# Kernel optimization log

Measured on AMD Instinct MI355X. Metric: run time of the kernel, lower is better.

## Reference

```python
import jax, jax.numpy as jnp
import numpy as np
from jax import lax

K = 3            # kernel size
KP = K * K       # kernel_size_prod
CENTER = KP // 2 # center tap index
PIXEL_SIZE = 1.0
DILATION = 1


def _unfold(x):
    # torch F.unfold equivalent: [N, C*KP, oh, ow] with channel-major, spatial-minor tap order
    return lax.conv_general_dilated_patches(
        x, filter_shape=(K, K), window_strides=(1, 1),
        padding=((1, 1), (1, 1)), rhs_dilation=(DILATION, DILATION))


def setup_inputs() -> dict:
    key = jax.random.key(0)
    ks = jax.random.split(key, 6)
    N, C, O, H, W = 8, 128, 128, 64, 64
    x = jax.random.normal(ks[0], (N, C, H, W), jnp.float32)
    depth = jax.random.uniform(ks[1], (N, 1, H, W), jnp.float32)  # >0 almost surely
    fx = jax.random.uniform(ks[2], (N,), jnp.float32) + 0.5       # per-image focal scale
    s = 1.0 / np.sqrt(C * KP)
    w0 = jax.random.normal(ks[3], (O, C, K, K), jnp.float32) * s
    w1 = jax.random.normal(ks[4], (O, C, K, K), jnp.float32) * s
    w2 = jax.random.normal(ks[5], (O, C, K, K), jnp.float32) * s
    return {"x": x, "depth": depth, "fx": fx, "w0": w0, "w1": w1, "w2": w2}


def reference(x, depth, fx, w0, w1, w2):
    N, C, H, W = x.shape
    O = w0.shape[0]
    patches = _unfold(x)                      # [N, C*9, oh, ow]
    oh, ow = patches.shape[2], patches.shape[3]
    L = oh * ow
    x_col = patches.reshape(N, C, KP, L)       # [N, C, 9, L]
    d_col = _unfold(depth).reshape(N, KP, L)   # [N, 9, L]

    valid = (d_col != 0.0).astype(jnp.float32)
    valid = valid * valid[:, CENTER:CENTER + 1, :]
    d_col = d_col * valid
    center = d_col[:, CENTER:CENTER + 1, :]    # [N, 1, L]
    grid = PIXEL_SIZE * DILATION * center / fx[:, None, None]
    half = grid * 0.5

    m0 = (jnp.abs(d_col - (center + grid)) <= half).astype(jnp.float32)
    m1 = (jnp.abs(d_col - center) <= half).astype(jnp.float32)
    m1 = jnp.clip(m1 + 1.0 - valid, 0.0, 1.0)
    m2 = (jnp.abs(d_col - (center - grid)) <= half).astype(jnp.float32)

    def branch(w, m):
        # (O, C*9) @ (N, C*9, L) as an einsum over (C, tap)
        return jnp.einsum('ock,nckl->nol', w.reshape(O, C, KP), x_col * m[:, None])

    out = branch(w0, m0) + branch(w1, m1) + branch(w2, m2)
    return out.reshape(N, O, oh, ow)
```

## Files before the change

### kernel.cpp

```cpp
#include <hip/hip_runtime.h>
#include <hip/hip_bf16.h>
#include <cstdint>
#include <cstddef>

#define Nn 8
#define Cc 128
#define Oo 128
#define Hh 64
#define Ww 64
#define LL (Hh * Ww)
#define KP 9

typedef __attribute__((ext_vector_type(8))) short short8;
typedef __attribute__((ext_vector_type(4))) float floatx4;
typedef __attribute__((ext_vector_type(4))) int intx4;

#define SGB(m, s, i) __builtin_amdgcn_sched_group_barrier(m, s, i)

__device__ __forceinline__ unsigned short f2bf(float f) {
  unsigned int u = __float_as_uint(f);
  u += 0x7fffu + ((u >> 16) & 1u);
  return (unsigned short)(u >> 16);
}

__global__ __launch_bounds__(256) void prep_all(const float* __restrict__ x,
                                                const float* __restrict__ w0,
                                                const float* __restrict__ w1,
                                                const float* __restrict__ w2,
                                                unsigned short* __restrict__ xt,
                                                unsigned short* __restrict__ wt2) {
  __shared__ float tile[Cc][Ww + 1];
  __shared__ unsigned short wl[Cc * KP];
  const int bid = blockIdx.x;
  const int t = threadIdx.x;
  if (bid < Nn * Hh) {
    const int n = bid >> 6;
    const int h = bid & 63;
    const float* src = x + (size_t)n * Cc * LL + (size_t)h * Ww;
#pragma unroll
    for (int it = 0; it < 8; ++it) {
      const int idx = t + it * 256;
      const int c = idx >> 4;
      const int w4 = (idx & 15) << 2;
      const float4 v = *reinterpret_cast<const float4*>(src + (size_t)c * LL + w4);
      tile[c][w4 + 0] = v.x; tile[c][w4 + 1] = v.y;
      tile[c][w4 + 2] = v.z; tile[c][w4 + 3] = v.w;
    }
    __syncthreads();
    unsigned short* dst = xt + (size_t)((n * Hh + h) * Ww) * Cc;
#pragma unroll
    for (int it = 0; it < 4; ++it) {
      const int idx = t + it * 256;
      const int w = idx >> 4;
      const int ch = (idx & 15) << 3;
      short8 v;
#pragma unroll
      for (int q = 0; q < 8; ++q)
        ((unsigned short*)&v)[q] = f2bf(tile[ch + q][w]);
      *reinterpret_cast<short8*>(dst + (size_t)w * Cc + ch) = v;
    }
  } else {
    const int bo = bid - Nn * Hh;
    const int b = bo >> 7;
    const int o = bo & 127;
    const float* w = (b == 0) ? w0 : (b == 1) ? w1 : w2;
    const float* src = w + (size_t)o * Cc * KP;
#pragma unroll
    for (int it = 0; it < 5; ++it) {
      const int idx = t + it * 256;
      if (idx < Cc * KP) wl[idx] = f2bf(src[idx]);
    }
    __syncthreads();
    const int obase = ((o >> 6) & 1) * 2048 + ((o >> 5) & 1) * 1024 +
                      ((o >> 4) & 1) * 512 + (o & 15) * 32;
#pragma unroll
    for (int it = 0; it < 5; ++it) {
      const int idx = t + it * 256;
      if (idx < Cc * KP) {
        const int kk = idx >> 7;
        const int c = idx & 127;
        const int c0 = c >> 5;
        const int cc = c & 31;
        wt2[(size_t)(b * 36 + kk * 4 + c0) * 4096 + obase + cc] = wl[c * KP + kk];
      }
    }
  }
}

#define LDXC 132
#define HALO_COLS 66
#define HALO_ROWS 4
#define NSTEP 36
#define BSTRIDE 147456

__global__ __launch_bounds__(256, 2) void conv_main(
    const unsigned short* __restrict__ xt,
    const unsigned short* __restrict__ wt2,
    const float* __restrict__ depth,
    const float* __restrict__ fx,
    float* __restrict__ out) {
  __shared__ unsigned short Xs[HALO_ROWS * HALO_COLS * LDXC];
  __shared__ unsigned int code32[128];

  const int g = blockIdx.x;
  const int n = g >> 6;
  const int rem = g & 63;
  const int pb = rem >> 1;
  const int ob1 = rem & 1;
  const int h0 = pb * 2;

  const int tid = threadIdx.x;
  const int lane = tid & 63;
  const int wave = tid >> 6;
  const int ln15 = lane & 15;
  const int quad = lane >> 4;
  const int hsel = wave >> 1;
  const int m_half = hsel * 64;
  const int wc = wave & 1;

  const unsigned short* wfrag = wt2 + (size_t)(ob1 * 2048 + wc * 1024 + ln15 * 32 + quad * 8);

  short8 Bb[4][6];
  short8 Aa[2][4];

#define LOADB(S)                                                                  \
  if ((S) < NSTEP) {                                                              \
    const unsigned short* bp = wfrag + (size_t)(S) * 4096;                        \
    Bb[(S) & 3][0] = *reinterpret_cast<const short8*>(bp);                        \
    Bb[(S) & 3][1] = *reinterpret_cast<const short8*>(bp + 512);                  \
    Bb[(S) & 3][2] = *reinterpret_cast<const short8*>(bp + BSTRIDE);              \
    Bb[(S) & 3][3] = *reinterpret_cast<const short8*>(bp + BSTRIDE + 512);        \
    Bb[(S) & 3][4] = *reinterpret_cast<const short8*>(bp + 2 * BSTRIDE);          \
    Bb[(S) & 3][5] = *reinterpret_cast<const short8*>(bp + 2 * BSTRIDE + 512);    \
  }

#define LOADA(S)                                                                  \
  if ((S) < NSTEP) {                                                              \
    const int kkp = (S) >> 2, c0p = (S) & 3;                                      \
    const int dyp = kkp / 3, dxp = kkp % 3;                                       \
    const int ab = ((hsel + dyp) * HALO_COLS + ln15 + dxp) * LDXC + quad * 8 + c0p * 32; \
    Aa[(S) & 1][0] = *reinterpret_cast<const short8*>(&Xs[ab]);                   \
    Aa[(S) & 1][1] = *reinterpret_cast<const short8*>(&Xs[ab + 16 * LDXC]);       \
    Aa[(S) & 1][2] = *reinterpret_cast<const short8*>(&Xs[ab + 32 * LDXC]);       \
    Aa[(S) & 1][3] = *reinterpret_cast<const short8*>(&Xs[ab + 48 * LDXC]);       \
  }

  LOADB(0)
  LOADB(1)
  LOADB(2)

#pragma unroll
  for (int it = 0; it < 17; ++it) {
    const int idx = tid + it * 256;
    if (idx < HALO_ROWS * HALO_COLS * 16) {
      const int ch = (idx & 15) << 3;
      const int pixidx = idx >> 4;
      const int lc = pixidx % HALO_COLS;
      const int hrel = pixidx / HALO_COLS;
      const int hh = h0 - 1 + hrel;
      const int ww = lc - 1;
      short8 v = {0, 0, 0, 0, 0, 0, 0, 0};
      if (hh >= 0 && hh < Hh && ww >= 0 && ww < Ww)
        v = *reinterpret_cast<const short8*>(
            xt + (size_t)((n * Hh + hh) * Ww + ww) * Cc + ch);
      *reinterpret_cast<short8*>(&Xs[pixidx * LDXC + ch]) = v;
    }
  }

  if (tid < 128) {
    const int m = tid;
    const int h = h0 + (m >> 6);
    const int w = m & 63;
    const float center = depth[n * LL + h * Ww + w];
    const float fxv = fx[n];
    const float grid = center / fxv;
    const float half = 0.5f * grid;
    unsigned int packed = 0u;
#pragma unroll
    for (int kk = 0; kk < KP; ++kk) {
      const int hh = h + kk / 3 - 1;
      const int ww = w + kk % 3 - 1;
      float d = 0.0f;
      if (hh >= 0 && hh < Hh && ww >= 0 && ww < Ww) d = depth[n * LL + hh * Ww + ww];
      const float valid = (d != 0.0f && center != 0.0f) ? 1.0f : 0.0f;
      const float dm = d * valid;
      unsigned int cb = 0u;
      if (fabsf(dm - (center + grid)) <= half) cb |= 1u;
      float m1v = (fabsf(dm - center) <= half) ? 1.0f : 0.0f;
      m1v = m1v + 1.0f - valid;
      if (m1v > 1.0f) m1v = 1.0f;
      if (m1v > 0.5f) cb |= 2u;
      if (fabsf(dm - (center - grid)) <= half) cb |= 4u;
      packed |= cb << (3 * kk);
    }
    code32[m] = packed;
  }

  __syncthreads();

  unsigned int cd[4];
#pragma unroll
  for (int i = 0; i < 4; ++i) cd[i] = code32[m_half + i * 16 + ln15];

  const floatx4 zf4 = {0.f, 0.f, 0.f, 0.f};
  floatx4 acc[4][2];
#pragma unroll
  for (int i = 0; i < 4; ++i)
#pragma unroll
    for (int j = 0; j < 2; ++j) acc[i][j] = zf4;

  LOADA(0)

#pragma unroll
  for (int s = 0; s < NSTEP; ++s) {
    LOADB(s + 3)
    LOADA(s + 1)
    const int kk = s >> 2;
    const int shift = 3 * kk;
    const short8* B = Bb[s & 3];
    const short8* A = Aa[s & 1];
#pragma unroll
    for (int b = 0; b < 3; ++b) {
#pragma unroll
      for (int i = 0; i < 4; ++i) {
        const int msk = __builtin_amdgcn_sbfe((int)cd[i], shift + b, 1);
        intx4 a4 = *reinterpret_cast<const intx4*>(&A[i]);
        intx4 m4 = {msk, msk, msk, msk};
        a4 &= m4;
        const short8 af = *reinterpret_cast<const short8*>(&a4);
        acc[i][0] = __builtin_amdgcn_mfma_f32_16x16x32_bf16(af, B[b * 2 + 0], acc[i][0], 0, 0, 0);
        acc[i][1] = __builtin_amdgcn_mfma_f32_16x16x32_bf16(af, B[b * 2 + 1], acc[i][1], 0, 0, 0);
      }
    }
    SGB(0x020, 2, 0); SGB(0x008, 4, 0);
    SGB(0x100, 2, 0); SGB(0x008, 4, 0);
    SGB(0x020, 2, 0); SGB(0x008, 4, 0);
    SGB(0x100, 2, 0); SGB(0x008, 4, 0);
    SGB(0x020, 2, 0); SGB(0x008, 8, 0);
  }

#pragma unroll
  for (int i = 0; i < 4; ++i) {
    const int m = m_half + i * 16 + quad * 4;
    const int h = h0 + (m >> 6);
    const int w = m & 63;
#pragma unroll
    for (int j = 0; j < 2; ++j) {
      const int o = ob1 * 64 + wc * 32 + j * 16 + ln15;
      float* dst = out + (size_t)(n * Oo + o) * LL + h * Ww + w;
      *reinterpret_cast<floatx4*>(dst) = acc[i][j];
    }
  }
}

extern "C" void kernel_launch(void* const* d_in, const int* in_sizes, int n_in,
                              void* d_out, int out_size, void* d_ws, size_t ws_size,
                              hipStream_t stream) {
  const float* x     = (const float*)d_in[0];
  const float* depth = (const float*)d_in[1];
  const float* fx    = (const float*)d_in[2];
  const float* w0    = (const float*)d_in[3];
  const float* w1    = (const float*)d_in[4];
  const float* w2    = (const float*)d_in[5];
  float* out = (float*)d_out;

  unsigned short* xt = (unsigned short*)d_ws;
  unsigned short* wt2 = xt + (size_t)Nn * Hh * Ww * Cc;

  prep_all<<<Nn * Hh + 3 * Oo, 256, 0, stream>>>(x, w0, w1, w2, xt, wt2);
  conv_main<<<512, 256, 0, stream>>>(xt, wt2, depth, fx, out);
}
```

Before: 117.6 us.

## Split K across waves with LDS reduction and precompute depth mask codes in prep

Moves the per-pixel depth mask code computation from conv_main into extra blocks of the prep kernel, writing packed codes to workspace. conv_main changes its wave decomposition: each wave now covers all 128 pixels of the tile and half of the channel reduction (split-K), which halves the B-fragment loads per wave and doubles A reuse. The two K halves are summed through LDS before the store. The cost is more accumulator registers (16 floatx4), an extra barrier, and an LDS reduction pass.

```diff
diff --git a/kernel.cpp b/kernel.cpp
--- a/kernel.cpp
+++ b/kernel.cpp
@@ -27,8 +27,11 @@
                                                 const float* __restrict__ w0,
                                                 const float* __restrict__ w1,
                                                 const float* __restrict__ w2,
+                                                const float* __restrict__ depth,
+                                                const float* __restrict__ fx,
                                                 unsigned short* __restrict__ xt,
-                                                unsigned short* __restrict__ wt2) {
+                                                unsigned short* __restrict__ wt2,
+                                                unsigned int* __restrict__ codesg) {
   __shared__ float tile[Cc][Ww + 1];
   __shared__ unsigned short wl[Cc * KP];
   const int bid = blockIdx.x;
@@ -59,7 +62,7 @@
         ((unsigned short*)&v)[q] = f2bf(tile[ch + q][w]);
       *reinterpret_cast<short8*>(dst + (size_t)w * Cc + ch) = v;
     }
-  } else {
+  } else if (bid < Nn * Hh + 3 * Oo) {
     const int bo = bid - Nn * Hh;
     const int b = bo >> 7;
     const int o = bo & 127;
@@ -84,23 +87,49 @@
         wt2[(size_t)(b * 36 + kk * 4 + c0) * 4096 + obase + cc] = wl[c * KP + kk];
       }
     }
+  } else {
+    const int p = (bid - (Nn * Hh + 3 * Oo)) * 256 + t;
+    const int n = p >> 12;
+    const int rem = p & 4095;
+    const int h = rem >> 6;
+    const int w = rem & 63;
+    const float center = depth[p];
+    const float grid = center / fx[n];
+    const float half = 0.5f * grid;
+    unsigned int packed = 0u;
+#pragma unroll
+    for (int kk = 0; kk < KP; ++kk) {
+      const int hh = h + kk / 3 - 1;
+      const int ww = w + kk % 3 - 1;
+      float d = 0.0f;
+      if (hh >= 0 && hh < Hh && ww >= 0 && ww < Ww) d = depth[(n << 12) + hh * Ww + ww];
+      const float valid = (d != 0.0f && center != 0.0f) ? 1.0f : 0.0f;
+      const float dm = d * valid;
+      unsigned int cb = 0u;
+      if (fabsf(dm - (center + grid)) <= half) cb |= 1u;
+      float m1v = (fabsf(dm - center) <= half) ? 1.0f : 0.0f;
+      m1v = m1v + 1.0f - valid;
+      if (m1v > 1.0f) m1v = 1.0f;
+      if (m1v > 0.5f) cb |= 2u;
+      if (fabsf(dm - (center - grid)) <= half) cb |= 4u;
+      packed |= cb << (3 * kk);
+    }
+    codesg[p] = packed;
   }
 }
 
 #define LDXC 132
 #define HALO_COLS 66
 #define HALO_ROWS 4
-#define NSTEP 36
+#define NSTEP 18
 #define BSTRIDE 147456
 
 __global__ __launch_bounds__(256, 2) void conv_main(
     const unsigned short* __restrict__ xt,
     const unsigned short* __restrict__ wt2,
-    const float* __restrict__ depth,
-    const float* __restrict__ fx,
+    const unsigned int* __restrict__ codesg,
     float* __restrict__ out) {
-  __shared__ unsigned short Xs[HALO_ROWS * HALO_COLS * LDXC];
-  __shared__ unsigned int code32[128];
+  __shared__ __align__(16) unsigned short Xs[HALO_ROWS * HALO_COLS * LDXC];
 
   const int g = blockIdx.x;
   const int n = g >> 6;
@@ -114,40 +143,60 @@
   const int wave = tid >> 6;
   const int ln15 = lane & 15;
   const int quad = lane >> 4;
-  const int hsel = wave >> 1;
-  const int m_half = hsel * 64;
   const int wc = wave & 1;
-
-  const unsigned short* wfrag = wt2 + (size_t)(ob1 * 2048 + wc * 1024 + ln15 * 32 + quad * 8);
-
-  short8 Bb[4][6];
-  short8 Aa[2][4];
-
-#define LOADB(S)                                                                  \
-  if ((S) < NSTEP) {                                                              \
-    const unsigned short* bp = wfrag + (size_t)(S) * 4096;                        \
-    Bb[(S) & 3][0] = *reinterpret_cast<const short8*>(bp);                        \
-    Bb[(S) & 3][1] = *reinterpret_cast<const short8*>(bp + 512);                  \
-    Bb[(S) & 3][2] = *reinterpret_cast<const short8*>(bp + BSTRIDE);              \
-    Bb[(S) & 3][3] = *reinterpret_cast<const short8*>(bp + BSTRIDE + 512);        \
-    Bb[(S) & 3][4] = *reinterpret_cast<const short8*>(bp + 2 * BSTRIDE);          \
-    Bb[(S) & 3][5] = *reinterpret_cast<const short8*>(bp + 2 * BSTRIDE + 512);    \
-  }
-
-#define LOADA(S)                                                                  \
-  if ((S) < NSTEP) {                                                              \
-    const int kkp = (S) >> 2, c0p = (S) & 3;                                      \
+  const int ks = wave >> 1;
+
+  const unsigned short* wfragk =
+      wt2 + (size_t)(ob1 * 2048 + wc * 1024 + ln15 * 32 + quad * 8) + (size_t)ks * 8192;
+  const int xbase = quad * 8 + ks * 64;
+
+  short8 Bb[3][6];
+  short8 Aa[2][8];
+
+#define LOADB(SLOT, S)                                                            \
+  {                                                                               \
+    const unsigned short* bp = wfragk + (size_t)((((S) >> 1) * 4) + ((S) & 1)) * 4096; \
+    Bb[SLOT][0] = *reinterpret_cast<const short8*>(bp);                           \
+    Bb[SLOT][1] = *reinterpret_cast<const short8*>(bp + 512);                     \
+    Bb[SLOT][2] = *reinterpret_cast<const short8*>(bp + BSTRIDE);                 \
+    Bb[SLOT][3] = *reinterpret_cast<const short8*>(bp + BSTRIDE + 512);           \
+    Bb[SLOT][4] = *reinterpret_cast<const short8*>(bp + 2 * BSTRIDE);             \
+    Bb[SLOT][5] = *reinterpret_cast<const short8*>(bp + 2 * BSTRIDE + 512);       \
+  }
+
+#define LOADA(SLOT, S)                                                            \
+  {                                                                               \
+    const int kkp = (S) >> 1;                                                     \
     const int dyp = kkp / 3, dxp = kkp % 3;                                       \
-    const int ab = ((hsel + dyp) * HALO_COLS + ln15 + dxp) * LDXC + quad * 8 + c0p * 32; \
-    Aa[(S) & 1][0] = *reinterpret_cast<const short8*>(&Xs[ab]);                   \
-    Aa[(S) & 1][1] = *reinterpret_cast<const short8*>(&Xs[ab + 16 * LDXC]);       \
-    Aa[(S) & 1][2] = *reinterpret_cast<const short8*>(&Xs[ab + 32 * LDXC]);       \
-    Aa[(S) & 1][3] = *reinterpret_cast<const short8*>(&Xs[ab + 48 * LDXC]);       \
-  }
-
-  LOADB(0)
-  LOADB(1)
-  LOADB(2)
+    _Pragma("unroll")                                                             \
+    for (int i = 0; i < 8; ++i) {                                                 \
+      const int off = (((i >> 2) + dyp) * HALO_COLS + (i & 3) * 16 + dxp) * LDXC  \
+                      + ((S) & 1) * 32;                                           \
+      Aa[SLOT][i] = *reinterpret_cast<const short8*>(&Xs[(ln15 + off) * 1 + xbase \
+                      + off - off + (ln15 * 0) + ((((i >> 2) + dyp) * HALO_COLS + (i & 3) * 16 + dxp + ln15) * LDXC + ((S) & 1) * 32 + xbase) - (ln15 + off + xbase)]); \
+    }                                                                             \
+  }
+#undef LOADA
+#define LOADA(SLOT, S)                                                            \
+  {                                                                               \
+    const int kkp = (S) >> 1;                                                     \
+    const int dyp = kkp / 3, dxp = kkp % 3;                                       \
+    _Pragma("unroll")                                                             \
+    for (int i = 0; i < 8; ++i) {                                                 \
+      const int pix = ((i >> 2) + dyp) * HALO_COLS + (i & 3) * 16 + ln15 + dxp;   \
+      Aa[SLOT][i] = *reinterpret_cast<const short8*>(&Xs[pix * LDXC + ((S) & 1) * 32 + xbase]); \
+    }                                                                             \
+  }
+
+  LOADB(0, 0)
+  LOADB(1, 1)
+
+  unsigned int cd[8];
+  {
+    const unsigned int* cp = codesg + (n << 12) + h0 * 64 + ln15;
+#pragma unroll
+    for (int i = 0; i < 8; ++i) cd[i] = cp[i * 16];
+  }
 
 #pragma unroll
   for (int it = 0; it < 17; ++it) {
@@ -167,62 +216,29 @@
     }
   }
 
-  if (tid < 128) {
-    const int m = tid;
-    const int h = h0 + (m >> 6);
-    const int w = m & 63;
-    const float center = depth[n * LL + h * Ww + w];
-    const float fxv = fx[n];
-    const float grid = center / fxv;
-    const float half = 0.5f * grid;
-    unsigned int packed = 0u;
-#pragma unroll
-    for (int kk = 0; kk < KP; ++kk) {
-      const int hh = h + kk / 3 - 1;
-      const int ww = w + kk % 3 - 1;
-      float d = 0.0f;
-      if (hh >= 0 && hh < Hh && ww >= 0 && ww < Ww) d = depth[n * LL + hh * Ww + ww];
-      const float valid = (d != 0.0f && center != 0.0f) ? 1.0f : 0.0f;
-      const float dm = d * valid;
-      unsigned int cb = 0u;
-      if (fabsf(dm - (center + grid)) <= half) cb |= 1u;
-      float m1v = (fabsf(dm - center) <= half) ? 1.0f : 0.0f;
-      m1v = m1v + 1.0f - valid;
-      if (m1v > 1.0f) m1v = 1.0f;
-      if (m1v > 0.5f) cb |= 2u;
-      if (fabsf(dm - (center - grid)) <= half) cb |= 4u;
-      packed |= cb << (3 * kk);
-    }
-    code32[m] = packed;
-  }
-
   __syncthreads();
 
-  unsigned int cd[4];
-#pragma unroll
-  for (int i = 0; i < 4; ++i) cd[i] = code32[m_half + i * 16 + ln15];
-
   const floatx4 zf4 = {0.f, 0.f, 0.f, 0.f};
-  floatx4 acc[4][2];
-#pragma unroll
-  for (int i = 0; i < 4; ++i)
+  floatx4 acc[8][2];
+#pragma unroll
+  for (int i = 0; i < 8; ++i)
 #pragma unroll
     for (int j = 0; j < 2; ++j) acc[i][j] = zf4;
 
-  LOADA(0)
+  LOADA(0, 0)
 
 #pragma unroll
   for (int s = 0; s < NSTEP; ++s) {
-    LOADB(s + 3)
-    LOADA(s + 1)
-    const int kk = s >> 2;
+    if (s + 2 < NSTEP) LOADB((s + 2) % 3, s + 2)
+    if (s + 1 < NSTEP) LOADA((s + 1) & 1, s + 1)
+    const int kk = s >> 1;
     const int shift = 3 * kk;
-    const short8* B = Bb[s & 3];
+    const short8* B = Bb[s % 3];
     const short8* A = Aa[s & 1];
 #pragma unroll
     for (int b = 0; b < 3; ++b) {
 #pragma unroll
-      for (int i = 0; i < 4; ++i) {
+      for (int i = 0; i < 8; ++i) {
         const int msk = __builtin_amdgcn_sbfe((int)cd[i], shift + b, 1);
         intx4 a4 = *reinterpret_cast<const intx4*>(&A[i]);
         intx4 m4 = {msk, msk, msk, msk};
@@ -232,23 +248,41 @@
         acc[i][1] = __builtin_amdgcn_mfma_f32_16x16x32_bf16(af, B[b * 2 + 1], acc[i][1], 0, 0, 0);
       }
     }
-    SGB(0x020, 2, 0); SGB(0x008, 4, 0);
-    SGB(0x100, 2, 0); SGB(0x008, 4, 0);
-    SGB(0x020, 2, 0); SGB(0x008, 4, 0);
-    SGB(0x100, 2, 0); SGB(0x008, 4, 0);
-    SGB(0x020, 2, 0); SGB(0x008, 8, 0);
-  }
-
-#pragma unroll
-  for (int i = 0; i < 4; ++i) {
-    const int m = m_half + i * 16 + quad * 4;
-    const int h = h0 + (m >> 6);
-    const int w = m & 63;
-#pragma unroll
-    for (int j = 0; j < 2; ++j) {
-      const int o = ob1 * 64 + wc * 32 + j * 16 + ln15;
-      float* dst = out + (size_t)(n * Oo + o) * LL + h * Ww + w;
-      *reinterpret_cast<floatx4*>(dst) = acc[i][j];
+    SGB(0x020, 1, 0); SGB(0x008, 4, 0); SGB(0x100, 1, 0); SGB(0x008, 4, 0);
+    SGB(0x020, 1, 0); SGB(0x008, 4, 0); SGB(0x100, 1, 0); SGB(0x008, 4, 0);
+    SGB(0x020, 1, 0); SGB(0x008, 4, 0); SGB(0x100, 1, 0); SGB(0x008, 4, 0);
+    SGB(0x020, 1, 0); SGB(0x008, 4, 0); SGB(0x100, 1, 0); SGB(0x008, 4, 0);
+    SGB(0x020, 1, 0); SGB(0x008, 4, 0); SGB(0x100, 1, 0); SGB(0x008, 4, 0);
+    SGB(0x020, 1, 0); SGB(0x008, 4, 0); SGB(0x100, 3, 0); SGB(0x008, 4, 0);
+  }
+
+  __syncthreads();
+  float* scratch = reinterpret_cast<float*>(Xs);
+  if (ks == 1) {
+#pragma unroll
+    for (int i = 0; i < 8; ++i)
+#pragma unroll
+      for (int j = 0; j < 2; ++j) {
+        const int tile = (wc * 16 + i * 2 + j) * 64 + lane;
+        *reinterpret_cast<floatx4*>(&scratch[tile * 4]) = acc[i][j];
+      }
+  }
+  __syncthreads();
+  if (ks == 0) {
+#pragma unroll
+    for (int i = 0; i < 8; ++i) {
+      const int m = i * 16 + quad * 4;
+      const int h = h0 + (m >> 6);
+      const int w = m & 63;
+#pragma unroll
+      for (int j = 0; j < 2; ++j) {
+        const int tile = (wc * 16 + i * 2 + j) * 64 + lane;
+        const floatx4 other = *reinterpret_cast<const floatx4*>(&scratch[tile * 4]);
+        const floatx4 sum = acc[i][j] + other;
+        const int o = ob1 * 64 + wc * 32 + j * 16 + ln15;
+        float* dst = out + (size_t)(n * Oo + o) * LL + h * Ww + w;
+        *reinterpret_cast<floatx4*>(dst) = sum;
+      }
     }
   }
 }
@@ -266,7 +300,8 @@
 
   unsigned short* xt = (unsigned short*)d_ws;
   unsigned short* wt2 = xt + (size_t)Nn * Hh * Ww * Cc;
-
-  prep_all<<<Nn * Hh + 3 * Oo, 256, 0, stream>>>(x, w0, w1, w2, xt, wt2);
-  conv_main<<<512, 256, 0, stream>>>(xt, wt2, depth, fx, out);
+  unsigned int* codesg = (unsigned int*)(wt2 + (size_t)3 * KP * Oo * Cc);
+
+  prep_all<<<Nn * Hh + 3 * Oo + 128, 256, 0, stream>>>(x, w0, w1, w2, depth, fx, xt, wt2, codesg);
+  conv_main<<<512, 256, 0, stream>>>(xt, wt2, codesg, out);
 }
```

Measured after the change: 109.6 us. -6.8%, faster.
